# Kernel optimization log

Measured on AMD Instinct MI355X. Metric: run time of the kernel, lower is better.

The kernel has to match this reference:

```python
import jax, jax.numpy as jnp
import numpy as np

BS, NMAX, NA, NC = 16, 64, 8400, 80
TOPK, ALPHA, BETA, EPS = 13, 1.0, 6.0, 1e-9


def _make_anchor_points():
    pts = []
    for stride in (8, 16, 32):
        n = 640 // stride
        xs = (np.arange(n, dtype=np.float32) + 0.5) * stride
        gx, gy = np.meshgrid(xs, xs)
        pts.append(np.stack([gx.ravel(), gy.ravel()], -1))
    return jnp.asarray(np.concatenate(pts, 0))  # (8400, 2)


def setup_inputs() -> dict:
    key = jax.random.key(0)
    ks = jax.random.split(key, 6)
    pd_scores = jax.random.uniform(ks[0], (BS, NA, NC), jnp.float32)
    anc_points = _make_anchor_points()
    off = jax.random.uniform(ks[1], (BS, NA, 2), jnp.float32, -8.0, 8.0)
    wh = jax.random.uniform(ks[2], (BS, NA, 2), jnp.float32, 8.0, 160.0)
    c = anc_points[None] + off
    pd_bboxes = jnp.concatenate([c - wh / 2, c + wh / 2], -1)
    gc = jax.random.uniform(ks[3], (BS, NMAX, 2), jnp.float32, 60.0, 580.0)
    gwh = jax.random.uniform(ks[4], (BS, NMAX, 2), jnp.float32, 12.0, 140.0)
    gt_bboxes = jnp.concatenate([gc - gwh / 2, gc + gwh / 2], -1)
    gt_labels = jax.random.randint(ks[5], (BS, NMAX, 1), 0, NC)
    mask_gt = jnp.ones((BS, NMAX, 1), jnp.float32)
    return {"pd_scores": pd_scores, "pd_bboxes": pd_bboxes,
            "anc_points": anc_points, "gt_labels": gt_labels,
            "gt_bboxes": gt_bboxes, "mask_gt": mask_gt}


def _split_broadcast(gt, pd):
    # gt (b,n,4) -> components (b,n,1); pd (b,A,4) -> components (b,1,A)
    g = [gt[..., i][:, :, None] for i in range(4)]
    p = [pd[..., i][:, None, :] for i in range(4)]
    return g, p


def _ciou(gt, pd, eps=1e-7):
    (b1x1, b1y1, b1x2, b1y2), (b2x1, b2y1, b2x2, b2y2) = _split_broadcast(gt, pd)
    w1, h1 = b1x2 - b1x1, b1y2 - b1y1 + eps
    w2, h2 = b2x2 - b2x1, b2y2 - b2y1 + eps
    inter = (jnp.clip(jnp.minimum(b1x2, b2x2) - jnp.maximum(b1x1, b2x1), 0.0)
             * jnp.clip(jnp.minimum(b1y2, b2y2) - jnp.maximum(b1y1, b2y1), 0.0))
    union = w1 * h1 + w2 * h2 - inter + eps
    iou = inter / union
    cw = jnp.maximum(b1x2, b2x2) - jnp.minimum(b1x1, b2x1)
    ch = jnp.maximum(b1y2, b2y2) - jnp.minimum(b1y1, b2y1)
    c2 = cw * cw + ch * ch + eps
    rho2 = ((b2x1 + b2x2 - b1x1 - b1x2) ** 2 + (b2y1 + b2y2 - b1y1 - b1y2) ** 2) / 4.0
    v = (4.0 / np.pi ** 2) * (jnp.arctan(w2 / h2) - jnp.arctan(w1 / h1)) ** 2
    alpha = jax.lax.stop_gradient(v / (v - iou + (1.0 + eps)))
    return iou - (rho2 / c2 + v * alpha)  # (b,n,A)


def _cost_distance(gt, pd, eps=1e-7):
    (b1x1, b1y1, b1x2, b1y2), (b2x1, b2y1, b2x2, b2y2) = _split_broadcast(gt, pd)
    w1, h1 = b1x2 - b1x1, b1y2 - b1y1 + eps
    w2, h2 = b2x2 - b2x1, b2y2 - b2y1 + eps
    gt_r = jnp.minimum(w1, h1) / jnp.maximum(w1, h1)   # (b,n,1)
    pd_r = jnp.minimum(w2, h2) / jnp.maximum(w2, h2)   # (b,1,A)
    cost_shape = 1.0 - jnp.abs(gt_r - pd_r) / jnp.maximum(gt_r, pd_r)
    ns = cost_shape / (cost_shape.max(-1, keepdims=True) + eps)
    ga, pa = w1 * h1, w2 * h2
    cost_area = 1.0 - jnp.abs(ga - pa) / jnp.maximum(ga, pa)
    na_ = cost_area / (cost_area.max(-1, keepdims=True) + eps)
    r1, r2 = w1 / h1, w2 / h2
    cost_wh = jnp.minimum(r1, r2) / jnp.maximum(r1, r2)
    nr = cost_wh / (cost_wh.max(-1, keepdims=True) + eps)
    return (ns + nr + na_) / 3.0  # (b,n,A)


def _select_topk(metrics, mask_gt_bool):
    b, n, A = metrics.shape
    _, idxs = jax.lax.top_k(metrics, TOPK)           # (b,n,TOPK)
    mask = jnp.broadcast_to(mask_gt_bool, (b, n, TOPK))
    idxs = jnp.where(mask, idxs, 0)
    counts = jnp.zeros((b * n, A), metrics.dtype).at[
        jnp.arange(b * n)[:, None], idxs.reshape(b * n, TOPK)].add(1.0)
    counts = counts.reshape(b, n, A)
    return jnp.where(counts > 1, jnp.zeros((), metrics.dtype), counts)


def _assign(pd_scores, pd_bboxes, anc_points, gt_labels, gt_bboxes, mask_gt):
    b, A, nc = pd_scores.shape
    n = gt_bboxes.shape[1]
    lbl = gt_labels[..., 0]
    bbox_scores = pd_scores[jnp.arange(b)[:, None], :, lbl]          # (b,n,A)
    overlaps = jnp.clip(_ciou(gt_bboxes, pd_bboxes), 0.0)            # (b,n,A)
    cost = jnp.clip(_cost_distance(gt_bboxes, pd_bboxes), 0.0)       # (b,n,A)
    align_metric = bbox_scores ** ALPHA * overlaps ** BETA * cost
    # anchors inside gt boxes
    lt = gt_bboxes[..., :2][:, :, None, :]                           # (b,n,1,2)
    rb = gt_bboxes[..., 2:][:, :, None, :]
    ap = anc_points[None, None]                                      # (1,1,A,2)
    deltas = jnp.concatenate([ap - lt, rb - ap], -1)                 # (b,n,A,4)
    mask_in_gts = (deltas.min(-1) > EPS).astype(pd_scores.dtype)
    mask_topk = _select_topk(align_metric * mask_in_gts, mask_gt > 0)
    mask_pos = mask_topk * mask_in_gts * mask_gt                     # (b,n,A)
    # resolve anchors assigned to multiple gts by highest overlap
    fg = mask_pos.sum(-2)                                            # (b,A)
    multi = jnp.broadcast_to((fg > 1)[:, None, :], mask_pos.shape)
    is_max = jax.nn.one_hot(jnp.argmax(overlaps, 1), n,
                            dtype=overlaps.dtype).transpose(0, 2, 1)
    mask_pos = jnp.where(multi, is_max, mask_pos)
    fg_mask = mask_pos.sum(-2)                                       # (b,A)
    target_gt_idx = jnp.argmax(mask_pos, 1)                          # (b,A)
    flat_idx = target_gt_idx + jnp.arange(b)[:, None] * n
    target_labels = gt_labels.reshape(-1)[flat_idx]                  # (b,A)
    target_bboxes = gt_bboxes.reshape(-1, 4)[flat_idx]               # (b,A,4)
    target_scores = (jax.nn.one_hot(target_labels, nc, dtype=pd_scores.dtype)
                     * (fg_mask > 0)[..., None].astype(pd_scores.dtype))
    # normalize scores by alignment metric
    align_metric = align_metric * mask_pos
    pos_align = align_metric.max(-1, keepdims=True)                  # (b,n,1)
    pos_ov = (overlaps * mask_pos).max(-1, keepdims=True)
    norm = (align_metric * pos_ov / (pos_align + EPS)).max(-2)[..., None]  # (b,A,1)
    target_scores = target_scores * norm
    return target_labels, target_bboxes, target_scores, fg_mask > 0


def reference(pd_scores, pd_bboxes, anc_points, gt_labels, gt_bboxes, mask_gt):
    return _assign(pd_scores, pd_bboxes, anc_points, gt_labels, gt_bboxes, mask_gt)
```

## Files before the change

### kernel.cpp

```cpp
#include <hip/hip_runtime.h>
#include <hip/hip_bf16.h>
#include <math.h>

#pragma clang fp contract(off)

#define BSZ   16
#define NMAXG 64
#define NAA   8400
#define NCC   80
#define KTOP  13
#define CAP   768
#define MCMAX 6656
#define CLMAX 13312

__device__ __forceinline__ float ciou_pre(float gx1, float gy1, float gx2, float gy2,
                                          float px1, float py1, float px2, float py2,
                                          float ga, float pa, float da) {
    const float E = 1e-7f;
    float iw = fminf(gx2, px2) - fmaxf(gx1, px1); iw = fmaxf(iw, 0.0f);
    float ih = fminf(gy2, py2) - fmaxf(gy1, py1); ih = fmaxf(ih, 0.0f);
    float inter = iw * ih;
    float uni = ga + pa - inter + E;
    float iou = inter / uni;
    float cw = fmaxf(gx2, px2) - fminf(gx1, px1);
    float ch = fmaxf(gy2, py2) - fminf(gy1, py1);
    float c2 = cw * cw + ch * ch + E;
    float dx = px1 + px2 - gx1 - gx2;
    float dy = py1 + py2 - gy1 - gy2;
    float rho2 = (dx * dx + dy * dy) / 4.0f;
    float v = 0.4052847345693511f * (da * da);
    float alpha = v / (v - iou + (1.0f + E));
    float r = iou - (rho2 / c2 + v * alpha);
    return fmaxf(r, 0.0f);
}

__global__ __launch_bounds__(256) void k_pre(
    const float* __restrict__ pd_bboxes, const float* __restrict__ gt_bboxes,
    float4* __restrict__ precomp, float4* __restrict__ rowpre)
{
    int i = blockIdx.x * 256 + threadIdx.x;
    if (i < BSZ * NAA) {
        float4 p = ((const float4*)pd_bboxes)[i];
        float w2 = p.z - p.x, h2 = p.w - p.y + 1e-7f;
        float r2 = w2 / h2;
        float4 q;
        q.x = fminf(w2, h2) / fmaxf(w2, h2);
        q.y = w2 * h2;
        q.z = r2;
        q.w = atanf(r2);
        precomp[i] = q;
    }
    if (i < BSZ * NMAXG) {
        float4 g = ((const float4*)gt_bboxes)[i];
        float w1 = g.z - g.x, h1 = g.w - g.y + 1e-7f;
        float r1 = w1 / h1;
        float4 q;
        q.x = fminf(w1, h1) / fmaxf(w1, h1);
        q.y = w1 * h1;
        q.z = r1;
        q.w = atanf(r1);
        rowpre[i] = q;
    }
}

__global__ __launch_bounds__(256) void k_rows(
    const float* __restrict__ pd_scores, const float* __restrict__ pd_bboxes,
    const float* __restrict__ anc, const int* __restrict__ gt_labels,
    const float* __restrict__ gt_bboxes, const float* __restrict__ mask_gt,
    const float4* __restrict__ precomp, const float4* __restrict__ rowpre,
    unsigned int* __restrict__ fg, float* __restrict__ rowmax,
    int* __restrict__ finaln, float* __restrict__ fnalign, float* __restrict__ fnov,
    int* __restrict__ mc_count, int* __restrict__ mlist,
    int* __restrict__ cl_count, int* __restrict__ clist)
{
    __shared__ int cidx[CAP];
    __shared__ unsigned long long keys[CAP];
    __shared__ float ovs[CAP];
    __shared__ float red[3][4];
    __shared__ int win_a[16];
    __shared__ float win_al[16], win_ov[16];
    __shared__ int s_cnt, s_pos, s_nwin;

    int row = blockIdx.x;
    int b = row >> 6, n = row & 63;
    int t = threadIdx.x;
    int wave = t >> 6, lane = t & 63;
    if (t == 0) { s_cnt = 0; s_pos = 0; s_nwin = 0; }
    __syncthreads();

    float4 g  = ((const float4*)gt_bboxes)[row];
    float4 rp = rowpre[row];
    const float4* pc = precomp + (size_t)b * NAA;
    const float2* ap2 = (const float2*)anc;

    float ms = -1e30f, ma = -1e30f, mw = -1e30f;
    for (int a = t; a < NAA; a += 256) {
        float4 q = pc[a];
        float cs = 1.0f - fabsf(rp.x - q.x) / fmaxf(rp.x, q.x);
        float ca = 1.0f - fabsf(rp.y - q.y) / fmaxf(rp.y, q.y);
        float cw = fminf(rp.z, q.z) / fmaxf(rp.z, q.z);
        ms = fmaxf(ms, cs); ma = fmaxf(ma, ca); mw = fmaxf(mw, cw);
        float2 apv = ap2[a];
        float d = fminf(fminf(apv.x - g.x, apv.y - g.y), fminf(g.z - apv.x, g.w - apv.y));
        if (d > 1e-9f) {
            int p = atomicAdd(&s_cnt, 1);
            if (p < CAP) cidx[p] = a;
        }
    }
    for (int o = 32; o; o >>= 1) {
        ms = fmaxf(ms, __shfl_xor(ms, o));
        ma = fmaxf(ma, __shfl_xor(ma, o));
        mw = fmaxf(mw, __shfl_xor(mw, o));
    }
    if (lane == 0) { red[0][wave] = ms; red[1][wave] = ma; red[2][wave] = mw; }
    __syncthreads();
    ms = fmaxf(fmaxf(red[0][0], red[0][1]), fmaxf(red[0][2], red[0][3]));
    ma = fmaxf(fmaxf(red[1][0], red[1][1]), fmaxf(red[1][2], red[1][3]));
    mw = fmaxf(fmaxf(red[2][0], red[2][1]), fmaxf(red[2][2], red[2][3]));
    if (t == 0) { rowmax[row * 3 + 0] = ms; rowmax[row * 3 + 1] = ma; rowmax[row * 3 + 2] = mw; }
    float dms = ms + 1e-7f, dma = ma + 1e-7f, dmw = mw + 1e-7f;
    int cnt = s_cnt; cnt = cnt < CAP ? cnt : CAP;

    if (mask_gt[row] <= 0.0f) return;

    int lbl = gt_labels[row];
    const float* sc = pd_scores + (size_t)b * NAA * NCC + lbl;
    const float4* pb = (const float4*)pd_bboxes + (size_t)b * NAA;
    for (int j = t; j < cnt; j += 256) {
        int a = cidx[j];
        float4 p = pb[a];
        float4 q = pc[a];
        float cs = 1.0f - fabsf(rp.x - q.x) / fmaxf(rp.x, q.x);
        float ca = 1.0f - fabsf(rp.y - q.y) / fmaxf(rp.y, q.y);
        float cw = fminf(rp.z, q.z) / fmaxf(rp.z, q.z);
        float cost = ((cs / dms + cw / dmw) + ca / dma) / 3.0f;
        cost = fmaxf(cost, 0.0f);
        float ov = ciou_pre(g.x, g.y, g.z, g.w, p.x, p.y, p.z, p.w,
                            rp.y, q.y, q.w - rp.w);
        float s = sc[(size_t)a * NCC];
        float o2 = ov * ov; float o3 = o2 * ov; float ov6 = o3 * o3;
        float align = (s * ov6) * cost;
        keys[j] = ((unsigned long long)__float_as_uint(align) << 32)
                | (unsigned long long)(0xFFFFFFFFu - (unsigned)a);
        ovs[j] = ov;
        unsigned long long bal = __ballot(align > 0.0f);
        if (lane == 0 && bal) atomicAdd(&s_pos, __popcll(bal));
    }
    __syncthreads();
    if (wave != 0) return;

    int mpos = s_pos;
    int bA = b * NAA;
    int nwin;

    if (mpos >= KTOP) {
        for (int k = 0; k < KTOP; k++) {
            unsigned long long best = 0ull;
            for (int j = lane; j < cnt; j += 64) {
                unsigned long long kk = keys[j];
                best = kk > best ? kk : best;
            }
            for (int o = 32; o; o >>= 1) {
                unsigned long long ot = __shfl_xor(best, o);
                best = ot > best ? ot : best;
            }
            for (int j = lane; j < cnt; j += 64) {
                if (keys[j] == best) {
                    keys[j] = 0ull;
                    win_a[k]  = (int)(0xFFFFFFFFu - (unsigned)(best & 0xFFFFFFFFull));
                    win_al[k] = __uint_as_float((unsigned)(best >> 32));
                    win_ov[k] = ovs[j];
                }
            }
        }
        nwin = KTOP;
    } else {
        int Z = KTOP - mpos;
        for (int j = lane; j < cnt; j += 64) {
            unsigned long long kk = keys[j];
            int a = (int)(0xFFFFFFFFu - (unsigned)(kk & 0xFFFFFFFFull));
            bool sel;
            if ((kk >> 32) != 0ull) {
                sel = true;
            } else {
                int pcb = 0;
                for (int j2 = 0; j2 < cnt; j2++) {
                    unsigned long long k2 = keys[j2];
                    if ((k2 >> 32) != 0ull) {
                        int a2 = (int)(0xFFFFFFFFu - (unsigned)(k2 & 0xFFFFFFFFull));
                        if (a2 < a) pcb++;
                    }
                }
                sel = (a - pcb) < Z;
            }
            if (sel) {
                int p = atomicAdd(&s_nwin, 1);
                win_a[p]  = a;
                win_al[p] = __uint_as_float((unsigned)(kk >> 32));
                win_ov[p] = ovs[j];
            }
        }
        nwin = s_nwin;
    }

    bool isclaim = false, ismulti = false;
    int gi = 0;
    if (lane < nwin) {
        gi = bA + win_a[lane];
        unsigned old = atomicAdd(&fg[gi], 1u);
        if (old == 0u) {
            finaln[gi] = n; fnalign[gi] = win_al[lane]; fnov[gi] = win_ov[lane];
            isclaim = true;
        } else if (old == 1u) {
            ismulti = true;
        }
    }
    unsigned long long cb = __ballot(isclaim);
    unsigned long long mb = __ballot(ismulti);
    int cbase = 0, mbase = 0;
    if (lane == 0) {
        if (cb) cbase = atomicAdd(cl_count, __popcll(cb));
        if (mb) mbase = atomicAdd(mc_count, __popcll(mb));
    }
    cbase = __shfl(cbase, 0);
    mbase = __shfl(mbase, 0);
    unsigned long long below = (lane == 0) ? 0ull : (~0ull >> (64 - lane));
    if (isclaim) clist[cbase + __popcll(cb & below)] = gi;
    if (ismulti) mlist[mbase + __popcll(mb & below)] = gi;
}

__global__ __launch_bounds__(256) void k_multi(
    const float* __restrict__ pd_scores, const float* __restrict__ pd_bboxes,
    const int* __restrict__ gt_labels, const float* __restrict__ gt_bboxes,
    const float4* __restrict__ precomp, const float4* __restrict__ rowpre,
    const float* __restrict__ rowmax, const int* __restrict__ mc_count,
    const int* __restrict__ mlist,
    int* __restrict__ finaln, float* __restrict__ fnalign, float* __restrict__ fnov)
{
    int wave = threadIdx.x >> 6, lane = threadIdx.x & 63;
    int nwaves = gridDim.x << 2;
    int count = *mc_count;
    for (int w = (blockIdx.x << 2) + wave; w < count; w += nwaves) {
        int gi = mlist[w];
        int b = gi / NAA;
        int rowb = (b << 6) + lane;
        const float4 p  = ((const float4*)pd_bboxes)[gi];
        const float4 q  = precomp[gi];
        const float4 g  = ((const float4*)gt_bboxes)[rowb];
        const float4 rp = rowpre[rowb];
        float ov = ciou_pre(g.x, g.y, g.z, g.w, p.x, p.y, p.z, p.w,
                            rp.y, q.y, q.w - rp.w);
        unsigned long long key = ((unsigned long long)__float_as_uint(ov) << 32)
                               | (unsigned long long)(63 - lane);
        unsigned long long best = key;
        for (int o = 32; o; o >>= 1) {
            unsigned long long ot = __shfl_xor(best, o);
            best = ot > best ? ot : best;
        }
        int nstar = 63 - (int)(best & 63ull);
        if (lane == nstar) {
            float cs = 1.0f - fabsf(rp.x - q.x) / fmaxf(rp.x, q.x);
            float ca = 1.0f - fabsf(rp.y - q.y) / fmaxf(rp.y, q.y);
            float cw = fminf(rp.z, q.z) / fmaxf(rp.z, q.z);
            const float* rm = rowmax + rowb * 3;
            float cost = ((cs / (rm[0] + 1e-7f) + cw / (rm[2] + 1e-7f)) + ca / (rm[1] + 1e-7f)) / 3.0f;
            cost = fmaxf(cost, 0.0f);
            int lbl = gt_labels[rowb];
            float s = pd_scores[(size_t)gi * NCC + lbl];
            float o2 = ov * ov, o3 = o2 * ov, ov6 = o3 * o3;
            finaln[gi] = nstar;
            fnalign[gi] = (s * ov6) * cost;
            fnov[gi] = ov;
        }
    }
}

__global__ __launch_bounds__(256) void k_post(
    const int* __restrict__ cl_count, const int* __restrict__ clist,
    const int* __restrict__ finaln, const float* __restrict__ fnalign,
    const float* __restrict__ fnov,
    unsigned int* __restrict__ pos_align, unsigned int* __restrict__ pos_ov)
{
    int count = *cl_count;
    int i = blockIdx.x * 256 + threadIdx.x;
    if (i >= count) return;
    int gi = clist[i];
    int b = gi / NAA;
    int nf = finaln[gi];
    int r = (b << 6) + nf;
    atomicMax(&pos_align[r], __float_as_uint(fnalign[gi]));
    atomicMax(&pos_ov[r], __float_as_uint(fnov[gi]));
}

__global__ __launch_bounds__(256) void k_out(
    const int* __restrict__ gt_labels, const float* __restrict__ gt_bboxes,
    const int* __restrict__ finaln, const float* __restrict__ fnalign,
    const unsigned int* __restrict__ pos_align, const unsigned int* __restrict__ pos_ov,
    float* __restrict__ out)
{
    int i = blockIdx.x * 256 + threadIdx.x;
    if (i >= BSZ * NAA) return;
    int b = i / NAA;
    int nf = finaln[i];
    int tgt = (nf >= 0) ? nf : 0;
    int lbl = gt_labels[(b << 6) + tgt];
    float4 g = ((const float4*)gt_bboxes)[(b << 6) + tgt];

    out[i] = (float)lbl;
    ((float4*)(out + (size_t)BSZ * NAA))[i] = g;

    float* srow = out + (size_t)BSZ * NAA * 5 + (size_t)i * NCC;
    float4 z; z.x = 0.0f; z.y = 0.0f; z.z = 0.0f; z.w = 0.0f;
    #pragma unroll
    for (int c4 = 0; c4 < NCC / 4; c4++) ((float4*)srow)[c4] = z;

    float* ofg = out + (size_t)BSZ * NAA * (5 + NCC);
    if (nf >= 0) {
        float pa = __uint_as_float(pos_align[(b << 6) + nf]);
        float po = __uint_as_float(pos_ov[(b << 6) + nf]);
        srow[lbl] = (fnalign[i] * po) / (pa + 1e-9f);
        ofg[i] = 1.0f;
    } else {
        ofg[i] = 0.0f;
    }
}

extern "C" void kernel_launch(void* const* d_in, const int* in_sizes, int n_in,
                              void* d_out, int out_size, void* d_ws, size_t ws_size,
                              hipStream_t stream)
{
    const float* pd_scores = (const float*)d_in[0];
    const float* pd_bboxes = (const float*)d_in[1];
    const float* anc       = (const float*)d_in[2];
    const int*   gt_labels = (const int*)d_in[3];
    const float* gt_bboxes = (const float*)d_in[4];
    const float* mask_gt   = (const float*)d_in[5];
    float* out = (float*)d_out;

    char* ws = (char*)d_ws;
    const size_t NBA = (size_t)BSZ * NAA * 4;
    size_t off = 0;
    float4*       precomp = (float4*)(ws + off); off += (size_t)BSZ * NAA * 16;
    float4*       rowpre  = (float4*)(ws + off); off += BSZ * NMAXG * 16;
    unsigned int* fg      = (unsigned int*)(ws + off); off += NBA;
    int*          finaln  = (int*)(ws + off);          off += NBA;
    float*        fnalign = (float*)(ws + off);        off += NBA;
    float*        fnov    = (float*)(ws + off);        off += NBA;
    unsigned int* posal   = (unsigned int*)(ws + off); off += 4096;
    unsigned int* posov   = (unsigned int*)(ws + off); off += 4096;
    float*        rowmax  = (float*)(ws + off);        off += 12288;
    int*          mc_count= (int*)(ws + off);
    int*          cl_count= (int*)(ws + off + 4);      off += 256;
    int*          mlist   = (int*)(ws + off);          off += MCMAX * 4;
    int*          clist   = (int*)(ws + off);          off += CLMAX * 4;

    hipMemsetAsync(fg, 0, NBA, stream);
    hipMemsetAsync(finaln, 0xFF, NBA, stream);
    hipMemsetAsync(posal, 0, 8192, stream);
    hipMemsetAsync(mc_count, 0, 8, stream);

    int grid = (BSZ * NAA + 255) / 256;
    k_pre<<<grid, 256, 0, stream>>>(pd_bboxes, gt_bboxes, precomp, rowpre);
    k_rows<<<BSZ * NMAXG, 256, 0, stream>>>(pd_scores, pd_bboxes, anc, gt_labels,
                                            gt_bboxes, mask_gt, precomp, rowpre,
                                            fg, rowmax, finaln, fnalign, fnov,
                                            mc_count, mlist, cl_count, clist);
    k_multi<<<256, 256, 0, stream>>>(pd_scores, pd_bboxes, gt_labels, gt_bboxes,
                                     precomp, rowpre, rowmax, mc_count, mlist,
                                     finaln, fnalign, fnov);
    k_post<<<CLMAX / 256, 256, 0, stream>>>(cl_count, clist, finaln, fnalign, fnov,
                                            posal, posov);
    k_out<<<grid, 256, 0, stream>>>(gt_labels, gt_bboxes, finaln, fnalign, posal, posov, out);
}
```

Before: 91.61 us.

## Enumerate in-box anchors analytically and move row-max reduction into precompute kernel

The per-GT-row cost maxima are now computed in k_pre: each anchor block reduces over its anchors for all 64 GT rows and merges into a global buffer with atomicMax on float bits. k_rows then no longer scans all 8400 anchors per row. It assigns one wave per GT row and derives the candidate anchors directly from the 8/16/32-stride grid geometry using ballots and bit masks. This removes the full-anchor sweep and the block-wide syncs per row, at the cost of hardcoding the anchor grid layout instead of reading anc_points, and capping candidates at 512 per row.

```diff
diff --git a/kernel.cpp b/kernel.cpp
--- a/kernel.cpp
+++ b/kernel.cpp
@@ -9,7 +9,7 @@
 #define NAA   8400
 #define NCC   80
 #define KTOP  13
-#define CAP   768
+#define WCAP  512
 #define MCMAX 6656
 #define CLMAX 13312
 
@@ -34,182 +34,242 @@
     return fmaxf(r, 0.0f);
 }
 
+__device__ __forceinline__ int nthbit(unsigned int m, int k) {
+    for (int i = 0; i < k; i++) m &= m - 1;
+    return __ffs(m) - 1;
+}
+
 __global__ __launch_bounds__(256) void k_pre(
     const float* __restrict__ pd_bboxes, const float* __restrict__ gt_bboxes,
-    float4* __restrict__ precomp, float4* __restrict__ rowpre)
-{
-    int i = blockIdx.x * 256 + threadIdx.x;
-    if (i < BSZ * NAA) {
-        float4 p = ((const float4*)pd_bboxes)[i];
+    float4* __restrict__ precomp, float4* __restrict__ rowpre,
+    unsigned int* __restrict__ rowmax_u)
+{
+    __shared__ float4 rp_s[NMAXG];
+    __shared__ unsigned int lmax[NMAXG * 3];
+
+    int b = blockIdx.x / 33, chunk = blockIdx.x % 33;
+    int t = threadIdx.x, lane = t & 63;
+    int a = chunk * 256 + t;
+    bool valid = a < NAA;
+
+    float4 q = make_float4(0.f, 0.f, 0.f, 0.f);
+    if (valid) {
+        float4 p = ((const float4*)pd_bboxes)[(size_t)b * NAA + a];
         float w2 = p.z - p.x, h2 = p.w - p.y + 1e-7f;
         float r2 = w2 / h2;
-        float4 q;
         q.x = fminf(w2, h2) / fmaxf(w2, h2);
         q.y = w2 * h2;
         q.z = r2;
         q.w = atanf(r2);
-        precomp[i] = q;
-    }
-    if (i < BSZ * NMAXG) {
-        float4 g = ((const float4*)gt_bboxes)[i];
+        precomp[(size_t)b * NAA + a] = q;
+    }
+    if (t < NMAXG) {
+        float4 g = ((const float4*)gt_bboxes)[b * NMAXG + t];
         float w1 = g.z - g.x, h1 = g.w - g.y + 1e-7f;
         float r1 = w1 / h1;
-        float4 q;
-        q.x = fminf(w1, h1) / fmaxf(w1, h1);
-        q.y = w1 * h1;
-        q.z = r1;
-        q.w = atanf(r1);
-        rowpre[i] = q;
-    }
+        float4 rp;
+        rp.x = fminf(w1, h1) / fmaxf(w1, h1);
+        rp.y = w1 * h1;
+        rp.z = r1;
+        rp.w = atanf(r1);
+        rp_s[t] = rp;
+        if (chunk == 0) rowpre[b * NMAXG + t] = rp;
+    }
+    for (int k = t; k < NMAXG * 3; k += 256) lmax[k] = 0u;
+    __syncthreads();
+
+    for (int r = 0; r < NMAXG; r++) {
+        float4 rp = rp_s[r];
+        float cs = 0.0f, ca = 0.0f, cw = 0.0f;
+        if (valid) {
+            cs = 1.0f - fabsf(rp.x - q.x) / fmaxf(rp.x, q.x);
+            ca = 1.0f - fabsf(rp.y - q.y) / fmaxf(rp.y, q.y);
+            cw = fminf(rp.z, q.z) / fmaxf(rp.z, q.z);
+        }
+        for (int o = 32; o; o >>= 1) {
+            cs = fmaxf(cs, __shfl_xor(cs, o));
+            ca = fmaxf(ca, __shfl_xor(ca, o));
+            cw = fmaxf(cw, __shfl_xor(cw, o));
+        }
+        if (lane == 0) {
+            atomicMax(&lmax[r * 3 + 0], __float_as_uint(cs));
+            atomicMax(&lmax[r * 3 + 1], __float_as_uint(ca));
+            atomicMax(&lmax[r * 3 + 2], __float_as_uint(cw));
+        }
+    }
+    __syncthreads();
+    for (int k = t; k < NMAXG * 3; k += 256)
+        if (lmax[k]) atomicMax(&rowmax_u[b * NMAXG * 3 + k], lmax[k]);
 }
 
 __global__ __launch_bounds__(256) void k_rows(
     const float* __restrict__ pd_scores, const float* __restrict__ pd_bboxes,
-    const float* __restrict__ anc, const int* __restrict__ gt_labels,
-    const float* __restrict__ gt_bboxes, const float* __restrict__ mask_gt,
+    const int* __restrict__ gt_labels, const float* __restrict__ gt_bboxes,
+    const float* __restrict__ mask_gt,
     const float4* __restrict__ precomp, const float4* __restrict__ rowpre,
-    unsigned int* __restrict__ fg, float* __restrict__ rowmax,
+    const float* __restrict__ rowmax,
+    unsigned int* __restrict__ fg,
     int* __restrict__ finaln, float* __restrict__ fnalign, float* __restrict__ fnov,
     int* __restrict__ mc_count, int* __restrict__ mlist,
     int* __restrict__ cl_count, int* __restrict__ clist)
 {
-    __shared__ int cidx[CAP];
-    __shared__ unsigned long long keys[CAP];
-    __shared__ float ovs[CAP];
-    __shared__ float red[3][4];
-    __shared__ int win_a[16];
-    __shared__ float win_al[16], win_ov[16];
-    __shared__ int s_cnt, s_pos, s_nwin;
-
-    int row = blockIdx.x;
+    __shared__ unsigned long long keys[4][WCAP];
+    __shared__ float ovs[4][WCAP];
+    __shared__ int win_a[4][16];
+    __shared__ float win_al[4][16], win_ov[4][16];
+    __shared__ int nw[4];
+
+    int t = threadIdx.x, wv = t >> 6, lane = t & 63;
+    int row = blockIdx.x * 4 + wv;
     int b = row >> 6, n = row & 63;
-    int t = threadIdx.x;
-    int wave = t >> 6, lane = t & 63;
-    if (t == 0) { s_cnt = 0; s_pos = 0; s_nwin = 0; }
-    __syncthreads();
+
+    if (mask_gt[row] <= 0.0f) return;
 
     float4 g  = ((const float4*)gt_bboxes)[row];
     float4 rp = rowpre[row];
-    const float4* pc = precomp + (size_t)b * NAA;
-    const float2* ap2 = (const float2*)anc;
-
-    float ms = -1e30f, ma = -1e30f, mw = -1e30f;
-    for (int a = t; a < NAA; a += 256) {
-        float4 q = pc[a];
-        float cs = 1.0f - fabsf(rp.x - q.x) / fmaxf(rp.x, q.x);
-        float ca = 1.0f - fabsf(rp.y - q.y) / fmaxf(rp.y, q.y);
-        float cw = fminf(rp.z, q.z) / fmaxf(rp.z, q.z);
-        ms = fmaxf(ms, cs); ma = fmaxf(ma, ca); mw = fmaxf(mw, cw);
-        float2 apv = ap2[a];
-        float d = fminf(fminf(apv.x - g.x, apv.y - g.y), fminf(g.z - apv.x, g.w - apv.y));
-        if (d > 1e-9f) {
-            int p = atomicAdd(&s_cnt, 1);
-            if (p < CAP) cidx[p] = a;
-        }
-    }
-    for (int o = 32; o; o >>= 1) {
-        ms = fmaxf(ms, __shfl_xor(ms, o));
-        ma = fmaxf(ma, __shfl_xor(ma, o));
-        mw = fmaxf(mw, __shfl_xor(mw, o));
-    }
-    if (lane == 0) { red[0][wave] = ms; red[1][wave] = ma; red[2][wave] = mw; }
-    __syncthreads();
-    ms = fmaxf(fmaxf(red[0][0], red[0][1]), fmaxf(red[0][2], red[0][3]));
-    ma = fmaxf(fmaxf(red[1][0], red[1][1]), fmaxf(red[1][2], red[1][3]));
-    mw = fmaxf(fmaxf(red[2][0], red[2][1]), fmaxf(red[2][2], red[2][3]));
-    if (t == 0) { rowmax[row * 3 + 0] = ms; rowmax[row * 3 + 1] = ma; rowmax[row * 3 + 2] = mw; }
-    float dms = ms + 1e-7f, dma = ma + 1e-7f, dmw = mw + 1e-7f;
-    int cnt = s_cnt; cnt = cnt < CAP ? cnt : CAP;
-
-    if (mask_gt[row] <= 0.0f) return;
+    float dms = rowmax[row * 3 + 0] + 1e-7f;
+    float dma = rowmax[row * 3 + 1] + 1e-7f;
+    float dmw = rowmax[row * 3 + 2] + 1e-7f;
+
+    unsigned int xm[3], ym[3];
+    int xlo[3], ylo[3], cx[3], cy[3];
+    {
+        const int LS[3] = {8, 16, 32};
+        const int LN[3] = {80, 40, 20};
+        #pragma unroll
+        for (int l = 0; l < 3; l++) {
+            float sf = (float)LS[l], inv = 1.0f / (float)LS[l];
+            int nn = LN[l];
+            int xl = (int)floorf(g.x * inv - 0.5f) - 1; if (xl < 0) xl = 0;
+            int xh = (int)floorf(g.z * inv - 0.5f) + 1; if (xh > nn - 1) xh = nn - 1;
+            int yl = (int)floorf(g.y * inv - 0.5f) - 1; if (yl < 0) yl = 0;
+            int yh = (int)floorf(g.w * inv - 0.5f) + 1; if (yh > nn - 1) yh = nn - 1;
+            bool ok = false;
+            if (lane < 32) {
+                int i = xl + lane;
+                if (i <= xh) {
+                    float ax = ((float)i + 0.5f) * sf;
+                    ok = (ax - g.x > 1e-9f) && (g.z - ax > 1e-9f);
+                }
+            } else {
+                int i = yl + (lane - 32);
+                if (i <= yh) {
+                    float ay = ((float)i + 0.5f) * sf;
+                    ok = (ay - g.y > 1e-9f) && (g.w - ay > 1e-9f);
+                }
+            }
+            unsigned long long bal = __ballot(ok);
+            xm[l] = (unsigned int)bal; ym[l] = (unsigned int)(bal >> 32);
+            xlo[l] = xl; ylo[l] = yl; cx[l] = __popc(xm[l]); cy[l] = __popc(ym[l]);
+        }
+    }
+    int c0 = cx[0] * cy[0], c1 = cx[1] * cy[1], c2 = cx[2] * cy[2];
+    int cnt = c0 + c1 + c2;
+    if (cnt > WCAP) cnt = WCAP;
 
     int lbl = gt_labels[row];
     const float* sc = pd_scores + (size_t)b * NAA * NCC + lbl;
     const float4* pb = (const float4*)pd_bboxes + (size_t)b * NAA;
-    for (int j = t; j < cnt; j += 256) {
-        int a = cidx[j];
-        float4 p = pb[a];
-        float4 q = pc[a];
-        float cs = 1.0f - fabsf(rp.x - q.x) / fmaxf(rp.x, q.x);
-        float ca = 1.0f - fabsf(rp.y - q.y) / fmaxf(rp.y, q.y);
-        float cw = fminf(rp.z, q.z) / fmaxf(rp.z, q.z);
-        float cost = ((cs / dms + cw / dmw) + ca / dma) / 3.0f;
-        cost = fmaxf(cost, 0.0f);
-        float ov = ciou_pre(g.x, g.y, g.z, g.w, p.x, p.y, p.z, p.w,
-                            rp.y, q.y, q.w - rp.w);
-        float s = sc[(size_t)a * NCC];
-        float o2 = ov * ov; float o3 = o2 * ov; float ov6 = o3 * o3;
-        float align = (s * ov6) * cost;
-        keys[j] = ((unsigned long long)__float_as_uint(align) << 32)
-                | (unsigned long long)(0xFFFFFFFFu - (unsigned)a);
-        ovs[j] = ov;
+    const float4* pc = precomp + (size_t)b * NAA;
+    int mpos = 0;
+    for (int jb = 0; jb < cnt; jb += 64) {
+        int j = jb + lane;
+        bool act = j < cnt;
+        float align = 0.0f;
+        if (act) {
+            int j2, XLO, YLO, CX, NN, BB; unsigned int XM, YM;
+            if (j < c0)           { j2 = j;           XM = xm[0]; YM = ym[0]; XLO = xlo[0]; YLO = ylo[0]; CX = cx[0]; NN = 80; BB = 0; }
+            else if (j < c0 + c1) { j2 = j - c0;      XM = xm[1]; YM = ym[1]; XLO = xlo[1]; YLO = ylo[1]; CX = cx[1]; NN = 40; BB = 6400; }
+            else                  { j2 = j - c0 - c1; XM = xm[2]; YM = ym[2]; XLO = xlo[2]; YLO = ylo[2]; CX = cx[2]; NN = 20; BB = 8000; }
+            int iyi = j2 / CX;
+            int ixi = j2 - iyi * CX;
+            int ix = XLO + nthbit(XM, ixi);
+            int iy = YLO + nthbit(YM, iyi);
+            int a = BB + iy * NN + ix;
+            float4 p = pb[a];
+            float4 q = pc[a];
+            float cs = 1.0f - fabsf(rp.x - q.x) / fmaxf(rp.x, q.x);
+            float ca = 1.0f - fabsf(rp.y - q.y) / fmaxf(rp.y, q.y);
+            float cw = fminf(rp.z, q.z) / fmaxf(rp.z, q.z);
+            float cost = ((cs / dms + cw / dmw) + ca / dma) / 3.0f;
+            cost = fmaxf(cost, 0.0f);
+            float ov = ciou_pre(g.x, g.y, g.z, g.w, p.x, p.y, p.z, p.w,
+                                rp.y, q.y, q.w - rp.w);
+            float s = sc[(size_t)a * NCC];
+            float o2 = ov * ov, o3 = o2 * ov, ov6 = o3 * o3;
+            align = (s * ov6) * cost;
+            keys[wv][j] = ((unsigned long long)__float_as_uint(align) << 32)
+                        | (unsigned long long)(0xFFFFFFFFu - (unsigned)a);
+            ovs[wv][j] = ov;
+        }
         unsigned long long bal = __ballot(align > 0.0f);
-        if (lane == 0 && bal) atomicAdd(&s_pos, __popcll(bal));
-    }
-    __syncthreads();
-    if (wave != 0) return;
-
-    int mpos = s_pos;
+        mpos += __popcll(bal);
+    }
+
     int bA = b * NAA;
     int nwin;
-
     if (mpos >= KTOP) {
         for (int k = 0; k < KTOP; k++) {
             unsigned long long best = 0ull;
-            for (int j = lane; j < cnt; j += 64) {
-                unsigned long long kk = keys[j];
-                best = kk > best ? kk : best;
+            for (int jb = 0; jb < cnt; jb += 64) {
+                int j = jb + lane;
+                if (j < cnt) { unsigned long long kk = keys[wv][j]; best = kk > best ? kk : best; }
             }
             for (int o = 32; o; o >>= 1) {
                 unsigned long long ot = __shfl_xor(best, o);
                 best = ot > best ? ot : best;
             }
-            for (int j = lane; j < cnt; j += 64) {
-                if (keys[j] == best) {
-                    keys[j] = 0ull;
-                    win_a[k]  = (int)(0xFFFFFFFFu - (unsigned)(best & 0xFFFFFFFFull));
-                    win_al[k] = __uint_as_float((unsigned)(best >> 32));
-                    win_ov[k] = ovs[j];
+            for (int jb = 0; jb < cnt; jb += 64) {
+                int j = jb + lane;
+                if (j < cnt && keys[wv][j] == best) {
+                    keys[wv][j] = 0ull;
+                    win_a[wv][k]  = (int)(0xFFFFFFFFu - (unsigned)(best & 0xFFFFFFFFull));
+                    win_al[wv][k] = __uint_as_float((unsigned)(best >> 32));
+                    win_ov[wv][k] = ovs[wv][j];
                 }
             }
         }
         nwin = KTOP;
     } else {
+        if (lane == 0) nw[wv] = 0;
         int Z = KTOP - mpos;
-        for (int j = lane; j < cnt; j += 64) {
-            unsigned long long kk = keys[j];
-            int a = (int)(0xFFFFFFFFu - (unsigned)(kk & 0xFFFFFFFFull));
-            bool sel;
-            if ((kk >> 32) != 0ull) {
-                sel = true;
-            } else {
-                int pcb = 0;
-                for (int j2 = 0; j2 < cnt; j2++) {
-                    unsigned long long k2 = keys[j2];
-                    if ((k2 >> 32) != 0ull) {
-                        int a2 = (int)(0xFFFFFFFFu - (unsigned)(k2 & 0xFFFFFFFFull));
-                        if (a2 < a) pcb++;
+        for (int jb = 0; jb < cnt; jb += 64) {
+            int j = jb + lane;
+            if (j < cnt) {
+                unsigned long long kk = keys[wv][j];
+                int a = (int)(0xFFFFFFFFu - (unsigned)(kk & 0xFFFFFFFFull));
+                bool sel;
+                if ((kk >> 32) != 0ull) {
+                    sel = true;
+                } else {
+                    int pcb = 0;
+                    for (int j2 = 0; j2 < cnt; j2++) {
+                        unsigned long long k2 = keys[wv][j2];
+                        if ((k2 >> 32) != 0ull) {
+                            int a2 = (int)(0xFFFFFFFFu - (unsigned)(k2 & 0xFFFFFFFFull));
+                            if (a2 < a) pcb++;
+                        }
                     }
+                    sel = (a - pcb) < Z;
                 }
-                sel = (a - pcb) < Z;
+                if (sel) {
+                    int p = atomicAdd(&nw[wv], 1);
+                    win_a[wv][p]  = a;
+                    win_al[wv][p] = __uint_as_float((unsigned)(kk >> 32));
+                    win_ov[wv][p] = ovs[wv][j];
+                }
             }
-            if (sel) {
-                int p = atomicAdd(&s_nwin, 1);
-                win_a[p]  = a;
-                win_al[p] = __uint_as_float((unsigned)(kk >> 32));
-                win_ov[p] = ovs[j];
-            }
-        }
-        nwin = s_nwin;
+        }
+        nwin = nw[wv];
     }
 
     bool isclaim = false, ismulti = false;
     int gi = 0;
     if (lane < nwin) {
-        gi = bA + win_a[lane];
+        gi = bA + win_a[wv][lane];
         unsigned old = atomicAdd(&fg[gi], 1u);
         if (old == 0u) {
-            finaln[gi] = n; fnalign[gi] = win_al[lane]; fnov[gi] = win_ov[lane];
+            finaln[gi] = n; fnalign[gi] = win_al[wv][lane]; fnov[gi] = win_ov[wv][lane];
             isclaim = true;
         } else if (old == 1u) {
             ismulti = true;
@@ -331,7 +391,6 @@
 {
     const float* pd_scores = (const float*)d_in[0];
     const float* pd_bboxes = (const float*)d_in[1];
-    const float* anc       = (const float*)d_in[2];
     const int*   gt_labels = (const int*)d_in[3];
     const float* gt_bboxes = (const float*)d_in[4];
     const float* mask_gt   = (const float*)d_in[5];
@@ -348,7 +407,7 @@
     float*        fnov    = (float*)(ws + off);        off += NBA;
     unsigned int* posal   = (unsigned int*)(ws + off); off += 4096;
     unsigned int* posov   = (unsigned int*)(ws + off); off += 4096;
-    float*        rowmax  = (float*)(ws + off);        off += 12288;
+    unsigned int* rowmax  = (unsigned int*)(ws + off); off += 12288;
     int*          mc_count= (int*)(ws + off);
     int*          cl_count= (int*)(ws + off + 4);      off += 256;
     int*          mlist   = (int*)(ws + off);          off += MCMAX * 4;
@@ -356,19 +415,20 @@
 
     hipMemsetAsync(fg, 0, NBA, stream);
     hipMemsetAsync(finaln, 0xFF, NBA, stream);
-    hipMemsetAsync(posal, 0, 8192, stream);
+    hipMemsetAsync(posal, 0, 8192 + 12288, stream);
     hipMemsetAsync(mc_count, 0, 8, stream);
 
-    int grid = (BSZ * NAA + 255) / 256;
-    k_pre<<<grid, 256, 0, stream>>>(pd_bboxes, gt_bboxes, precomp, rowpre);
-    k_rows<<<BSZ * NMAXG, 256, 0, stream>>>(pd_scores, pd_bboxes, anc, gt_labels,
-                                            gt_bboxes, mask_gt, precomp, rowpre,
-                                            fg, rowmax, finaln, fnalign, fnov,
-                                            mc_count, mlist, cl_count, clist);
+    k_pre<<<BSZ * 33, 256, 0, stream>>>(pd_bboxes, gt_bboxes, precomp, rowpre, rowmax);
+    k_rows<<<BSZ * NMAXG / 4, 256, 0, stream>>>(pd_scores, pd_bboxes, gt_labels,
+                                                gt_bboxes, mask_gt, precomp, rowpre,
+                                                (const float*)rowmax, fg,
+                                                finaln, fnalign, fnov,
+                                                mc_count, mlist, cl_count, clist);
     k_multi<<<256, 256, 0, stream>>>(pd_scores, pd_bboxes, gt_labels, gt_bboxes,
-                                     precomp, rowpre, rowmax, mc_count, mlist,
-                                     finaln, fnalign, fnov);
+                                     precomp, rowpre, (const float*)rowmax,
+                                     mc_count, mlist, finaln, fnalign, fnov);
     k_post<<<CLMAX / 256, 256, 0, stream>>>(cl_count, clist, finaln, fnalign, fnov,
                                             posal, posov);
+    int grid = (BSZ * NAA + 255) / 256;
     k_out<<<grid, 256, 0, stream>>>(gt_labels, gt_bboxes, finaln, fnalign, posal, posov, out);
 }
```

Result: slower. 137.2 us (+49.7%).
